# Kernel tuning notes

Hardware: AMD Instinct MI355X
Metric: run time of the kernel (lower is better)

Reference implementation:

```python
import jax, jax.numpy as jnp
import numpy as np

TEMP = 0.05
EPS = 1e-8  # torch CosineSimilarity eps


def setup_inputs() -> dict:
    key = jax.random.key(0)
    k1, k2, k3 = jax.random.split(key, 3)
    N, D = 4096, 1024
    c = jax.random.normal(k1, (N, D), dtype=jnp.float32)
    ch = jax.random.normal(k2, (N, D), dtype=jnp.float32)
    m_label = jax.random.randint(k3, (N,), 0, 64)
    return {"c": c, "ch": ch, "m_label": m_label}


def reference(c, ch, m_label):
    # Cosine similarity via normalization + GEMM (avoids [N,N,D] broadcast intermediate)
    cn = c / jnp.maximum(jnp.linalg.norm(c, axis=-1, keepdims=True), EPS)
    chn = ch / jnp.maximum(jnp.linalg.norm(ch, axis=-1, keepdims=True), EPS)
    sim = jnp.einsum('id,jd->ij', cn, chn) / TEMP  # [N, N]

    y_true = (m_label[:, None] == m_label[None, :]).astype(jnp.int32)
    mask = y_true.astype(sim.dtype)

    # SupCon-style masked softmax loss (logits_mask == 1 in source -> diagonal kept)
    logits = sim - jax.lax.stop_gradient(jnp.max(sim, axis=1, keepdims=True))
    log_prob = logits - jnp.log(jnp.sum(jnp.exp(logits), axis=1, keepdims=True))
    mean_log_prob_pos = jnp.sum(mask * log_prob, axis=1) / jnp.sum(mask, axis=1)
    loss = -jnp.mean(mean_log_prob_pos)

    return sim * TEMP, loss, y_true
```

## Files before the change

### kernel.cpp

```cpp
#include <hip/hip_runtime.h>
#include <hip/hip_bf16.h>

typedef __attribute__((ext_vector_type(8))) short short8;
typedef __attribute__((ext_vector_type(4))) float f32x4;

static constexpr int N = 4096;
static constexpr int D = 1024;
#define TEMP_INV 20.0f
#define LOG2E_X20 28.8539008178f

#define GLD_LDS16(gp, lp) __builtin_amdgcn_global_load_lds(                      \
    (const __attribute__((address_space(1))) void*)(gp),                         \
    (__attribute__((address_space(3))) void*)(lp), 16, 0, 0)

__global__ __launch_bounds__(256) void normalize_k(
    const float* __restrict__ c, const float* __restrict__ ch,
    unsigned short* __restrict__ cnb, unsigned short* __restrict__ chnb,
    float* __restrict__ loss_slot) {
  const int r = blockIdx.x;
  const int t = threadIdx.x;
  if (r == 0 && t == 0) *loss_slot = 0.0f;

  const float* src = (r < N) ? (c + (size_t)r * D) : (ch + (size_t)(r - N) * D);
  unsigned short* dst = (r < N) ? (cnb + (size_t)r * D) : (chnb + (size_t)(r - N) * D);

  float4 v = ((const float4*)src)[t];
  float ss = v.x * v.x + v.y * v.y + v.z * v.z + v.w * v.w;
  #pragma unroll
  for (int off = 32; off > 0; off >>= 1) ss += __shfl_xor(ss, off);
  __shared__ float red[4];
  if ((t & 63) == 0) red[t >> 6] = ss;
  __syncthreads();
  float tot = red[0] + red[1] + red[2] + red[3];
  float sc = 1.0f / fmaxf(sqrtf(tot), 1e-8f);

  __hip_bfloat16 b0 = __float2bfloat16(v.x * sc);
  __hip_bfloat16 b1 = __float2bfloat16(v.y * sc);
  __hip_bfloat16 b2 = __float2bfloat16(v.z * sc);
  __hip_bfloat16 b3 = __float2bfloat16(v.w * sc);
  ushort4 o;
  o.x = *(unsigned short*)&b0;
  o.y = *(unsigned short*)&b1;
  o.z = *(unsigned short*)&b2;
  o.w = *(unsigned short*)&b3;
  ((ushort4*)dst)[t] = o;
}

__global__ __launch_bounds__(256) void ytrue_k(
    const int* __restrict__ lbl, float* __restrict__ yt) {
  const size_t base = (size_t)blockIdx.x * 1024;
  const int row = (int)(base >> 12);
  const int lr = lbl[row];
  #pragma unroll
  for (int q = 0; q < 4; ++q) {
    const size_t e = base + q * 256 + threadIdx.x;
    const int col = (int)(e & 4095);
    yt[e] = (lbl[col] == lr) ? 1.0f : 0.0f;
  }
}

__global__ __launch_bounds__(512) void gemm_k(
    const unsigned short* __restrict__ A,
    const unsigned short* __restrict__ B,
    const int* __restrict__ lbl,
    float* __restrict__ sim, float* __restrict__ part) {
  __shared__ __align__(16) unsigned short Als[2][256 * 64];
  __shared__ __align__(16) unsigned short Bls[2][256 * 64];

  const int t = threadIdx.x;
  const int w = t >> 6, l = t & 63;
  const int bm = blockIdx.y, bn = blockIdx.x;
  const int wm = w >> 2, wn = w & 3;

  f32x4 acc[8][4] = {};

  const unsigned short* ga0 = A + (size_t)(bm * 256 + (t >> 3)) * D + (t & 7) * 8;
  const unsigned short* gb0 = B + (size_t)(bn * 256 + (t >> 3)) * D + (t & 7) * 8;

  const int frow = (l & 15);
  const int fk = (l >> 4) * 8;

#define STAGE(bb, ks) do {                                                     \
    const int _k = (ks) * 64;                                                  \
    _Pragma("unroll")                                                          \
    for (int q = 0; q < 4; ++q) {                                              \
      GLD_LDS16(ga0 + (size_t)q * 64 * D + _k, &Als[bb][q * 4096 + w * 512]);  \
      GLD_LDS16(gb0 + (size_t)q * 64 * D + _k, &Bls[bb][q * 4096 + w * 512]);  \
    }                                                                          \
  } while (0)

#define COMPUTE(bb) do {                                                       \
    _Pragma("unroll")                                                          \
    for (int ksub = 0; ksub < 2; ++ksub) {                                     \
      short8 af[8], bf[4];                                                     \
      _Pragma("unroll")                                                        \
      for (int m = 0; m < 8; ++m)                                              \
        af[m] = *(const short8*)&Als[bb][(wm * 128 + m * 16 + frow) * 64 +     \
                                         ksub * 32 + fk];                      \
      _Pragma("unroll")                                                        \
      for (int n = 0; n < 4; ++n)                                              \
        bf[n] = *(const short8*)&Bls[bb][(wn * 64 + n * 16 + frow) * 64 +      \
                                         ksub * 32 + fk];                      \
      _Pragma("unroll")                                                        \
      for (int m = 0; m < 8; ++m)                                              \
        _Pragma("unroll")                                                      \
        for (int n = 0; n < 4; ++n)                                            \
          acc[m][n] = __builtin_amdgcn_mfma_f32_16x16x32_bf16(af[m], bf[n],    \
                                                          acc[m][n], 0, 0, 0); \
    }                                                                          \
  } while (0)

  STAGE(0, 0);
  __syncthreads();

  for (int kk = 0; kk < 7; ++kk) {
    STAGE(1, 2 * kk + 1);
    COMPUTE(0);
    __syncthreads();
    STAGE(0, 2 * kk + 2);
    COMPUTE(1);
    __syncthreads();
  }
  STAGE(1, 15);
  COMPUTE(0);
  __syncthreads();
  COMPUTE(1);
#undef STAGE
#undef COMPUTE

  const int row0 = bm * 256 + wm * 128;
  const int col0 = bn * 256 + wn * 64;
  const int tile = bn * 4 + wn;
  int lc[4];
  #pragma unroll
  for (int n = 0; n < 4; ++n) lc[n] = lbl[col0 + n * 16 + (l & 15)];

  #pragma unroll
  for (int m = 0; m < 8; ++m) {
    #pragma unroll
    for (int r = 0; r < 4; ++r) {
      const int grow = row0 + m * 16 + (l >> 4) * 4 + r;
      const int lr = lbl[grow];
      const size_t base = (size_t)grow * N + col0 + (l & 15);
      float s = 0.0f, p = 0.0f;
      #pragma unroll
      for (int n = 0; n < 4; ++n) {
        const float v = acc[m][n][r];
        sim[base + n * 16] = v;
        s += exp2f(v * LOG2E_X20);
        p += (lc[n] == lr) ? v : 0.0f;
      }
      #pragma unroll
      for (int off = 1; off < 16; off <<= 1) {
        s += __shfl_xor(s, off);
        p += __shfl_xor(p, off);
      }
      if ((l & 15) == 0) {
        float* pp = &part[(size_t)grow * 128 + tile * 2];
        pp[0] = s;
        pp[1] = p;
      }
    }
  }
}

__global__ __launch_bounds__(256) void finalize_k(
    const float* __restrict__ part, const int* __restrict__ lbl,
    float* loss_slot) {
  __shared__ int hist[64];
  __shared__ float redl[4];
  const int t = threadIdx.x;
  const int i = blockIdx.x * 256 + t;

  if (t < 64) hist[t] = 0;
  __syncthreads();
  for (int j = t; j < N; j += 256) atomicAdd(&hist[lbl[j] & 63], 1);
  __syncthreads();

  const float* pr = part + (size_t)i * 128;
  float sexp = 0.0f, psum = 0.0f;
  #pragma unroll
  for (int tt = 0; tt < 64; ++tt) {
    sexp += pr[tt * 2];
    psum += pr[tt * 2 + 1];
  }
  const float cnt = (float)hist[lbl[i] & 63];
  const float row = TEMP_INV * psum / cnt - logf(sexp);
  float contrib = -row * (1.0f / (float)N);

  #pragma unroll
  for (int off = 32; off > 0; off >>= 1) contrib += __shfl_xor(contrib, off);
  if ((t & 63) == 0) redl[t >> 6] = contrib;
  __syncthreads();
  if (t == 0) atomicAdd(loss_slot, redl[0] + redl[1] + redl[2] + redl[3]);
}

extern "C" void kernel_launch(void* const* d_in, const int* in_sizes, int n_in,
                              void* d_out, int out_size, void* d_ws, size_t ws_size,
                              hipStream_t stream) {
  const float* c  = (const float*)d_in[0];
  const float* ch = (const float*)d_in[1];
  const int* lbl  = (const int*)d_in[2];

  float* out = (float*)d_out;
  float* sim = out;
  float* loss_slot = out + (size_t)N * N;
  float* ytrue = out + (size_t)N * N + 1;

  unsigned short* cnb  = (unsigned short*)d_ws;
  unsigned short* chnb = cnb + (size_t)N * D;
  float* part = (float*)(chnb + (size_t)N * D);

  normalize_k<<<2 * N, 256, 0, stream>>>(c, ch, cnb, chnb, loss_slot);
  ytrue_k<<<N * N / 1024, 256, 0, stream>>>(lbl, ytrue);
  dim3 g(N / 256, N / 256);
  gemm_k<<<g, 512, 0, stream>>>(cnb, chnb, lbl, sim, part);
  finalize_k<<<N / 256, 256, 0, stream>>>(part, lbl, loss_slot);
}
```

Baseline: 217.1 us.

## Triple-buffer GEMM K-loop with 32-wide stages, LDS swizzle, and vmcnt waits

Result: no change. 214.0 us (-1.4%).

```diff
diff --git a/kernel.cpp b/kernel.cpp
--- a/kernel.cpp
+++ b/kernel.cpp
@@ -64,8 +64,8 @@
     const unsigned short* __restrict__ B,
     const int* __restrict__ lbl,
     float* __restrict__ sim, float* __restrict__ part) {
-  __shared__ __align__(16) unsigned short Als[2][256 * 64];
-  __shared__ __align__(16) unsigned short Bls[2][256 * 64];
+  __shared__ __align__(16) unsigned short Als[3][256 * 32];
+  __shared__ __align__(16) unsigned short Bls[3][256 * 32];
 
   const int t = threadIdx.x;
   const int w = t >> 6, l = t & 63;
@@ -74,59 +74,63 @@
 
   f32x4 acc[8][4] = {};
 
-  const unsigned short* ga0 = A + (size_t)(bm * 256 + (t >> 3)) * D + (t & 7) * 8;
-  const unsigned short* gb0 = B + (size_t)(bn * 256 + (t >> 3)) * D + (t & 7) * 8;
+  const int srow = t >> 2;
+  const int sslot = (t & 3) ^ ((t >> 3) & 3);
+  const unsigned short* gaS = A + (size_t)(bm * 256 + srow) * D + sslot * 8;
+  const unsigned short* gbS = B + (size_t)(bn * 256 + srow) * D + sslot * 8;
 
   const int frow = (l & 15);
   const int fk = (l >> 4) * 8;
+  const int rswz = ((frow >> 1) & 3) << 3;
 
 #define STAGE(bb, ks) do {                                                     \
-    const int _k = (ks) * 64;                                                  \
+    const int _k = (ks) * 32;                                                  \
+    GLD_LDS16(gaS + _k, &Als[bb][w * 512]);                                    \
+    GLD_LDS16(gaS + (size_t)128 * D + _k, &Als[bb][4096 + w * 512]);           \
+    GLD_LDS16(gbS + _k, &Bls[bb][w * 512]);                                    \
+    GLD_LDS16(gbS + (size_t)128 * D + _k, &Bls[bb][4096 + w * 512]);           \
+  } while (0)
+
+#define COMPUTE(bb) do {                                                       \
+    short8 af[8], bf[4];                                                       \
     _Pragma("unroll")                                                          \
-    for (int q = 0; q < 4; ++q) {                                              \
-      GLD_LDS16(ga0 + (size_t)q * 64 * D + _k, &Als[bb][q * 4096 + w * 512]);  \
-      GLD_LDS16(gb0 + (size_t)q * 64 * D + _k, &Bls[bb][q * 4096 + w * 512]);  \
-    }                                                                          \
-  } while (0)
-
-#define COMPUTE(bb) do {                                                       \
+    for (int m = 0; m < 8; ++m)                                                \
+      af[m] = *(const short8*)&Als[bb][(wm * 128 + m * 16 + frow) * 32 +       \
+                                       (fk ^ rswz)];                           \
     _Pragma("unroll")                                                          \
-    for (int ksub = 0; ksub < 2; ++ksub) {                                     \
-      short8 af[8], bf[4];                                                     \
-      _Pragma("unroll")                                                        \
-      for (int m = 0; m < 8; ++m)                                              \
-        af[m] = *(const short8*)&Als[bb][(wm * 128 + m * 16 + frow) * 64 +     \
-                                         ksub * 32 + fk];                      \
+    for (int n = 0; n < 4; ++n)                                                \
+      bf[n] = *(const short8*)&Bls[bb][(wn * 64 + n * 16 + frow) * 32 +        \
+                                       (fk ^ rswz)];                           \
+    __builtin_amdgcn_s_setprio(1);                                             \
+    _Pragma("unroll")                                                          \
+    for (int m = 0; m < 8; ++m)                                                \
       _Pragma("unroll")                                                        \
       for (int n = 0; n < 4; ++n)                                              \
-        bf[n] = *(const short8*)&Bls[bb][(wn * 64 + n * 16 + frow) * 64 +      \
-                                         ksub * 32 + fk];                      \
-      _Pragma("unroll")                                                        \
-      for (int m = 0; m < 8; ++m)                                              \
-        _Pragma("unroll")                                                      \
-        for (int n = 0; n < 4; ++n)                                            \
-          acc[m][n] = __builtin_amdgcn_mfma_f32_16x16x32_bf16(af[m], bf[n],    \
-                                                          acc[m][n], 0, 0, 0); \
-    }                                                                          \
+        acc[m][n] = __builtin_amdgcn_mfma_f32_16x16x32_bf16(af[m], bf[n],      \
+                                                        acc[m][n], 0, 0, 0);   \
+    __builtin_amdgcn_s_setprio(0);                                             \
   } while (0)
 
+#define ITER(K, CUR, VM) do {                                                  \
+    if ((K) < 30) STAGE(((CUR) + 2) % 3, (K) + 2);                             \
+    asm volatile("s_waitcnt vmcnt(" #VM ")" ::: "memory");                     \
+    __builtin_amdgcn_s_barrier();                                              \
+    COMPUTE(CUR);                                                              \
+    __builtin_amdgcn_s_barrier();                                              \
+  } while (0)
+
   STAGE(0, 0);
-  __syncthreads();
-
-  for (int kk = 0; kk < 7; ++kk) {
-    STAGE(1, 2 * kk + 1);
-    COMPUTE(0);
-    __syncthreads();
-    STAGE(0, 2 * kk + 2);
-    COMPUTE(1);
-    __syncthreads();
-  }
-  STAGE(1, 15);
-  COMPUTE(0);
-  __syncthreads();
-  COMPUTE(1);
+  STAGE(1, 1);
+  for (int kb = 0; kb < 30; kb += 3) {
+    ITER(kb + 0, 0, 8);
+    ITER(kb + 1, 1, 8);
+    ITER(kb + 2, 2, 8);
+  }
+  ITER(30, 0, 4);
+  ITER(31, 1, 0);
 #undef STAGE
 #undef COMPUTE
+#undef ITER
 
   const int row0 = bm * 256 + wm * 128;
   const int col0 = bn * 256 + wn * 64;
```
